# Kernel optimization log

Measured on AMD Instinct MI355X. Metric: run time of the kernel, lower is better.

Reference implementation:

```python
import jax, jax.numpy as jnp
import numpy as np

H = 8
D = 512  # dmodel; each naive head projects to full D (not D//H)


def setup_inputs() -> dict:
    key = jax.random.key(0)
    ks = jax.random.split(key, 9)
    s = 1.0 / np.sqrt(D)
    x = jax.random.normal(ks[0], (2, 2048, D), dtype=jnp.float32)
    Wq = jax.random.normal(ks[1], (H, D, D), dtype=jnp.float32) * s
    Wk = jax.random.normal(ks[2], (H, D, D), dtype=jnp.float32) * s
    Wv = jax.random.normal(ks[3], (H, D, D), dtype=jnp.float32) * s
    bq = jnp.zeros((H, D), dtype=jnp.float32)
    bk = jnp.zeros((H, D), dtype=jnp.float32)
    bv = jnp.zeros((H, D), dtype=jnp.float32)
    Wo = jax.random.normal(ks[4], (H * D, D), dtype=jnp.float32) * (1.0 / np.sqrt(H * D))
    bo = jnp.zeros((D,), dtype=jnp.float32)
    return {"x": x, "Wq": Wq, "Wk": Wk, "Wv": Wv, "bq": bq, "bk": bk, "bv": bv, "Wo": Wo, "bo": bo}


def reference(x, Wq, Wk, Wv, bq, bk, bv, Wo, bo):
    # Batched form of the per-head Python loop: q/k/v -> [b, h, s, d]
    q = jnp.einsum("bsd,hde->bhse", x, Wq) + bq[None, :, None, :]
    k = jnp.einsum("bsd,hde->bhse", x, Wk) + bk[None, :, None, :]
    v = jnp.einsum("bsd,hde->bhse", x, Wv) + bv[None, :, None, :]
    scale = 1.0 / jnp.sqrt(jnp.asarray(D, dtype=x.dtype))
    scores = jnp.einsum("bhqe,bhke->bhqk", q, k) * scale  # [b, h, s, s]
    attn = jax.nn.softmax(scores, axis=-1)
    heads = jnp.einsum("bhqk,bhke->bhqe", attn, v)  # [b, h, s, d]
    b, h, s, d = heads.shape
    concat = jnp.transpose(heads, (0, 2, 1, 3)).reshape(b, s, h * d)  # concat on last axis
    out = concat @ Wo + bo  # output projection
    return out + x  # residual add
```

## Files before the change

### kernel.cpp

```cpp
#include <hip/hip_runtime.h>

typedef unsigned short u16;
typedef __attribute__((ext_vector_type(8))) short bh8;
typedef __attribute__((ext_vector_type(4))) float f32x4;
typedef __attribute__((ext_vector_type(4))) u16 us4;
typedef __attribute__((ext_vector_type(8))) u16 us8;

__device__ __forceinline__ u16 f2bf(float f){
  unsigned u = __builtin_bit_cast(unsigned, f);
  u += 0x7fffu + ((u >> 16) & 1u);
  return (u16)(u >> 16);
}
__device__ __forceinline__ float bf2f(u16 b){
  unsigned u = ((unsigned)b) << 16;
  return __builtin_bit_cast(float, u);
}

__device__ __forceinline__ void gload16(const void* g, void* l){
  __builtin_amdgcn_global_load_lds((const __attribute__((address_space(1))) unsigned*)g,
                                   (__attribute__((address_space(3))) unsigned*)l, 16, 0, 0);
}

template<int OUT_MODE>
__device__ __forceinline__ void gemm_core(
    u16* As, u16* Bs,
    const u16* __restrict__ A, int lda,
    const u16* __restrict__ B, int ldb,
    int K, float scale,
    const float* __restrict__ bias,
    const float* __restrict__ resid, int ldr,
    float* __restrict__ outF, u16* __restrict__ outB, int ldo,
    int m0, int n0)
{
  const int t  = threadIdx.x;
  const int ln = t & 63;
  const int wv = t >> 6;
  const int wr = wv >> 1;
  const int wc = wv & 1;

  const int rs = t >> 2;
  const int cs = (t & 3) * 8;
  const u16* Ag0 = A + (size_t)(m0 + rs) * lda + cs;
  const u16* Ag1 = Ag0 + (size_t)64 * lda;
  const u16* Bg0 = B + (size_t)(n0 + rs) * ldb + cs;
  const u16* Bg1 = Bg0 + (size_t)64 * ldb;
  char* lA0 = (char*)As + wv * 1024;
  char* lA1 = lA0 + 4096;
  char* lB0 = (char*)Bs + wv * 1024;
  char* lB1 = lB0 + 4096;

  f32x4 acc[4][4] = {};

  const int frow = (ln & 15);
  const int fk   = (ln >> 4) * 8;

  for (int k0 = 0; k0 < K; k0 += 32){
    gload16(Ag0 + k0, lA0);
    gload16(Ag1 + k0, lA1);
    gload16(Bg0 + k0, lB0);
    gload16(Bg1 + k0, lB1);
    __syncthreads();
    bh8 a[4], b[4];
#pragma unroll
    for (int i = 0; i < 4; i++)
      a[i] = *(const bh8*)&As[(wr*64 + i*16 + frow)*32 + fk];
#pragma unroll
    for (int j = 0; j < 4; j++)
      b[j] = *(const bh8*)&Bs[(wc*64 + j*16 + frow)*32 + fk];
#pragma unroll
    for (int i = 0; i < 4; i++)
#pragma unroll
      for (int j = 0; j < 4; j++)
        acc[i][j] = __builtin_amdgcn_mfma_f32_16x16x32_bf16(a[i], b[j], acc[i][j], 0, 0, 0);
    __syncthreads();
  }

  const int col0 = ln & 15;
  const int r0   = (ln >> 4) * 4;
#pragma unroll
  for (int i = 0; i < 4; i++){
    const int rowb = m0 + wr*64 + i*16 + r0;
#pragma unroll
    for (int j = 0; j < 4; j++){
      const int col = n0 + wc*64 + j*16 + col0;
      f32x4 v = acc[i][j];
      const float bb = bias ? bias[col] : 0.f;
      if (OUT_MODE == 0){
#pragma unroll
        for (int q = 0; q < 4; q++){
          float o = v[q] * scale + bb;
          if (resid) o += resid[(size_t)(rowb + q) * ldr + col];
          outF[(size_t)(rowb + q) * ldo + col] = o;
        }
      } else if (OUT_MODE == 1){
#pragma unroll
        for (int q = 0; q < 4; q++)
          outB[(size_t)(rowb + q) * ldo + col] = f2bf(v[q] * scale + bb);
      } else {
        us4 pk;
#pragma unroll
        for (int q = 0; q < 4; q++) pk[q] = f2bf(v[q] * scale + bb);
        *(us4*)&outB[(size_t)col * ldo + rowb] = pk;
      }
    }
  }
}


__global__ __launch_bounds__(256) void k_qkv_qk(
    const u16* __restrict__ xb, const u16* __restrict__ WT,
    const float* __restrict__ bq, const float* __restrict__ bk,
    u16* __restrict__ Q, u16* __restrict__ Kb)
{
  __shared__ u16 As[4096], Bs[4096];
  const int z = blockIdx.z;
  const int p = z >> 4, bh = z & 15, b = bh >> 3, h = bh & 7;
  const u16* A = xb + (size_t)b * 2048 * 512;
  const u16* B = WT + (size_t)(p * 8 + h) * 512 * 512;
  const float* bias = (p == 0 ? bq : bk) + h * 512;
  u16* out = (p == 0 ? Q : Kb) + (size_t)bh * 2048 * 512;
  gemm_core<1>(As, Bs, A, 512, B, 512, 512, 1.f, bias, nullptr, 0,
               nullptr, out, 512, blockIdx.y * 128, blockIdx.x * 128);
}

__global__ __launch_bounds__(256) void k_qkv_v(
    const u16* __restrict__ xb, const u16* __restrict__ WT,
    const float* __restrict__ bv, u16* __restrict__ VT)
{
  __shared__ u16 As[4096], Bs[4096];
  const int bh = blockIdx.z, b = bh >> 3, h = bh & 7;
  const u16* A = xb + (size_t)b * 2048 * 512;
  const u16* B = WT + (size_t)(16 + h) * 512 * 512;
  gemm_core<2>(As, Bs, A, 512, B, 512, 512, 1.f, bv + h * 512, nullptr, 0,
               nullptr, VT + (size_t)bh * 512 * 2048, 2048,
               blockIdx.y * 128, blockIdx.x * 128);
}

__global__ __launch_bounds__(256) void k_score(
    const u16* __restrict__ Q, const u16* __restrict__ Kb,
    u16* __restrict__ scoresB, int bh0)
{
  __shared__ u16 As[4096], Bs[4096];
  const int z = blockIdx.z, bh = bh0 + z;
  gemm_core<1>(As, Bs, Q + (size_t)bh * 2048 * 512, 512,
               Kb + (size_t)bh * 2048 * 512, 512, 512,
               0.044194173824159216f , nullptr, nullptr, 0,
               nullptr, scoresB + (size_t)z * 2048 * 2048, 2048,
               blockIdx.y * 128, blockIdx.x * 128);
}

__global__ __launch_bounds__(256) void k_softmax(u16* __restrict__ scoresB)
{
  u16* row = scoresB + (size_t)blockIdx.x * 2048;
  const int t = threadIdx.x, ln = t & 63, wv = t >> 6;
  us8 in = *(const us8*)(row + t * 8);
  float vals[8];
#pragma unroll
  for (int q = 0; q < 8; q++) vals[q] = bf2f(in[q]);
  float m = vals[0];
#pragma unroll
  for (int q = 1; q < 8; q++) m = fmaxf(m, vals[q]);
#pragma unroll
  for (int off = 32; off; off >>= 1) m = fmaxf(m, __shfl_xor(m, off));
  __shared__ float redm[4], reds[4];
  if (ln == 0) redm[wv] = m;
  __syncthreads();
  m = fmaxf(fmaxf(redm[0], redm[1]), fmaxf(redm[2], redm[3]));
  float e[8], s = 0.f;
#pragma unroll
  for (int q = 0; q < 8; q++){ e[q] = __expf(vals[q] - m); s += e[q]; }
#pragma unroll
  for (int off = 32; off; off >>= 1) s += __shfl_xor(s, off);
  if (ln == 0) reds[wv] = s;
  __syncthreads();
  s = reds[0] + reds[1] + reds[2] + reds[3];
  const float inv = 1.f / s;
  us8 pk;
#pragma unroll
  for (int q = 0; q < 8; q++) pk[q] = f2bf(e[q] * inv);
  *(us8*)(row + t * 8) = pk;
}

__global__ __launch_bounds__(256) void k_pv(
    const u16* __restrict__ scoresB, const u16* __restrict__ VT,
    u16* __restrict__ concat, int bh0)
{
  __shared__ u16 As[4096], Bs[4096];
  const int z = blockIdx.z, bh = bh0 + z, b = bh >> 3, h = bh & 7;
  gemm_core<1>(As, Bs, scoresB + (size_t)z * 2048 * 2048, 2048,
               VT + (size_t)bh * 512 * 2048, 2048, 2048, 1.f, nullptr, nullptr, 0,
               nullptr, concat + (size_t)b * 2048 * 4096 + h * 512, 4096,
               blockIdx.y * 128, blockIdx.x * 128);
}

__global__ __launch_bounds__(256) void k_final_sk(
    const u16* __restrict__ concat, const u16* __restrict__ WoT,
    float* __restrict__ partial)
{
  __shared__ u16 As[4096], Bs[4096];
  const int sk = blockIdx.z;
  gemm_core<0>(As, Bs, concat + sk * 1024, 4096,
               WoT + sk * 1024, 4096, 1024, 1.f, nullptr, nullptr, 0,
               partial + (size_t)sk * 4096 * 512, nullptr, 512,
               blockIdx.y * 128, blockIdx.x * 128);
}

__global__ __launch_bounds__(256) void k_reduce(
    const float* __restrict__ partial, const float* __restrict__ bo,
    const float* __restrict__ x, float* __restrict__ out)
{
  const size_t i4 = ((size_t)blockIdx.x * 256 + threadIdx.x) * 4;
  const int col = (int)(i4 & 511);
  float4 s = *(const float4*)(x + i4);
  s.x += bo[col]; s.y += bo[col + 1]; s.z += bo[col + 2]; s.w += bo[col + 3];
#pragma unroll
  for (int sk = 0; sk < 4; sk++){
    float4 p = *(const float4*)(partial + (size_t)sk * 2097152 + i4);
    s.x += p.x; s.y += p.y; s.z += p.z; s.w += p.w;
  }
  *(float4*)(out + i4) = s;
}


__global__ void k_convx(const float* __restrict__ x, u16* __restrict__ xb)
{
  const int i = blockIdx.x * blockDim.x + threadIdx.x;
  float4 v = *(const float4*)(x + (size_t)i * 4);
  us4 o; o[0] = f2bf(v.x); o[1] = f2bf(v.y); o[2] = f2bf(v.z); o[3] = f2bf(v.w);
  *(us4*)(xb + (size_t)i * 4) = o;
}

__global__ void k_transpose_f2b(const float* __restrict__ in, u16* __restrict__ out,
                                int rows, int cols, size_t inStride, size_t outStride)
{
  __shared__ float tile[32][33];
  const float* ip = in + blockIdx.z * inStride;
  u16* op = out + blockIdx.z * outStride;
  const int c0 = blockIdx.x * 32, r0 = blockIdx.y * 32;
  const int tx = threadIdx.x, ty = threadIdx.y;
#pragma unroll
  for (int m = 0; m < 4; m++)
    tile[ty + m * 8][tx] = ip[(size_t)(r0 + ty + m * 8) * cols + c0 + tx];
  __syncthreads();
#pragma unroll
  for (int m = 0; m < 4; m++)
    op[(size_t)(c0 + ty + m * 8) * rows + r0 + tx] = f2bf(tile[tx][ty + m * 8]);
}


extern "C" void kernel_launch(void* const* d_in, const int* in_sizes, int n_in,
                              void* d_out, int out_size, void* d_ws, size_t ws_size,
                              hipStream_t stream)
{
  const float* x  = (const float*)d_in[0];
  const float* Wq = (const float*)d_in[1];
  const float* Wk = (const float*)d_in[2];
  const float* Wv = (const float*)d_in[3];
  const float* bq = (const float*)d_in[4];
  const float* bk = (const float*)d_in[5];
  const float* bv = (const float*)d_in[6];
  const float* Wo = (const float*)d_in[7];
  const float* bo = (const float*)d_in[8];
  float* out = (float*)d_out;

  char* w = (char*)d_ws;
  size_t off = 0;
  auto alloc = [&](size_t bytes) -> char* {
    char* p = w + off; off += (bytes + 255) & ~(size_t)255; return p;
  };
  u16* xb   = (u16*)alloc(4096ull * 512 * 2);
  u16* WT   = (u16*)alloc(3ull * 8 * 512 * 512 * 2);
  u16* WoT  = (u16*)alloc(512ull * 4096 * 2);
  u16* Q    = (u16*)alloc(16ull * 2048 * 512 * 2);
  u16* Kb   = (u16*)alloc(16ull * 2048 * 512 * 2);
  u16* VT   = (u16*)alloc(16ull * 512 * 2048 * 2);
  u16* conc = (u16*)alloc(4096ull * 4096 * 2);
  float* part = (float*)alloc(4ull * 4096 * 512 * 4);
  const size_t scoreBytes = 2048ull * 2048 * 2;
  int CH = 16;
  while (CH > 1 && off + (size_t)CH * scoreBytes > ws_size) CH >>= 1;
  u16* scores = (u16*)alloc((size_t)CH * scoreBytes);

  k_convx<<<2048, 256, 0, stream>>>(x, xb);
  dim3 tb(32, 8);
  k_transpose_f2b<<<dim3(16, 16, 8), tb, 0, stream>>>(Wq, WT + 0ull * 2097152, 512, 512, 262144, 262144);
  k_transpose_f2b<<<dim3(16, 16, 8), tb, 0, stream>>>(Wk, WT + 1ull * 2097152, 512, 512, 262144, 262144);
  k_transpose_f2b<<<dim3(16, 16, 8), tb, 0, stream>>>(Wv, WT + 2ull * 2097152, 512, 512, 262144, 262144);
  k_transpose_f2b<<<dim3(16, 128, 1), tb, 0, stream>>>(Wo, WoT, 4096, 512, 0, 0);

  k_qkv_qk<<<dim3(4, 16, 32), 256, 0, stream>>>(xb, WT, bq, bk, Q, Kb);
  k_qkv_v <<<dim3(4, 16, 16), 256, 0, stream>>>(xb, WT, bv, VT);

  for (int c = 0; c < 16; c += CH){
    k_score  <<<dim3(16, 16, CH), 256, 0, stream>>>(Q, Kb, scores, c);
    k_softmax<<<dim3(CH * 2048), 256, 0, stream>>>(scores);
    k_pv     <<<dim3(4, 16, CH), 256, 0, stream>>>(scores, VT, conc, c);
  }

  k_final_sk<<<dim3(4, 32, 4), 256, 0, stream>>>(conc, WoT, part);
  k_reduce<<<2048, 256, 0, stream>>>(part, bo, x, out);
}
```

Measured before the change: 494.7 us.

## Fuse softmax into score GEMM epilogue with atomic row sums, defer normalization to PV

The score GEMM epilogue now writes exp(scaled score) directly and atomically accumulates per-row sums, and the PV GEMM divides by those sums in its epilogue. This removes the separate softmax kernel and its full read/write pass over the score matrix. It skips max-subtraction, so it relies on scores being small enough not to overflow exp. The split-K partials of the output projection are stored as bf16 instead of fp32 to halve their traffic, and the three QKV weight transposes are merged into one launch.

After: 465.6 us. 5.9% less time.

```diff
diff --git a/kernel.cpp b/kernel.cpp
--- a/kernel.cpp
+++ b/kernel.cpp
@@ -28,8 +28,9 @@
     const u16* __restrict__ B, int ldb,
     int K, float scale,
     const float* __restrict__ bias,
-    const float* __restrict__ resid, int ldr,
-    float* __restrict__ outF, u16* __restrict__ outB, int ldo,
+    float* __restrict__ lsum,
+    const float* __restrict__ lraw,
+    u16* __restrict__ outB, int ldo,
     int m0, int n0)
 {
   const int t  = threadIdx.x;
@@ -77,30 +78,51 @@
 
   const int col0 = ln & 15;
   const int r0   = (ln >> 4) * 4;
+  float rsum[4][4];
 #pragma unroll
   for (int i = 0; i < 4; i++){
     const int rowb = m0 + wr*64 + i*16 + r0;
+#pragma unroll
+    for (int q = 0; q < 4; q++) rsum[i][q] = 0.f;
 #pragma unroll
     for (int j = 0; j < 4; j++){
       const int col = n0 + wc*64 + j*16 + col0;
       f32x4 v = acc[i][j];
-      const float bb = bias ? bias[col] : 0.f;
-      if (OUT_MODE == 0){
-#pragma unroll
-        for (int q = 0; q < 4; q++){
-          float o = v[q] * scale + bb;
-          if (resid) o += resid[(size_t)(rowb + q) * ldr + col];
-          outF[(size_t)(rowb + q) * ldo + col] = o;
-        }
-      } else if (OUT_MODE == 1){
+      if (OUT_MODE == 1){
+        const float bb = bias ? bias[col] : 0.f;
 #pragma unroll
         for (int q = 0; q < 4; q++)
           outB[(size_t)(rowb + q) * ldo + col] = f2bf(v[q] * scale + bb);
-      } else {
+      } else if (OUT_MODE == 2){
+        const float bb = bias ? bias[col] : 0.f;
         us4 pk;
 #pragma unroll
         for (int q = 0; q < 4; q++) pk[q] = f2bf(v[q] * scale + bb);
         *(us4*)&outB[(size_t)col * ldo + rowb] = pk;
+      } else if (OUT_MODE == 3){
+#pragma unroll
+        for (int q = 0; q < 4; q++){
+          float e = __expf(v[q] * scale);
+          rsum[i][q] += e;
+          outB[(size_t)(rowb + q) * ldo + col] = f2bf(e);
+        }
+      } else {
+#pragma unroll
+        for (int q = 0; q < 4; q++){
+          float il = 1.0f / lraw[rowb + q];
+          outB[(size_t)(rowb + q) * ldo + col] = f2bf(v[q] * il);
+        }
+      }
+    }
+    if (OUT_MODE == 3){
+#pragma unroll
+      for (int q = 0; q < 4; q++){
+        float s = rsum[i][q];
+        s += __shfl_xor(s, 1);
+        s += __shfl_xor(s, 2);
+        s += __shfl_xor(s, 4);
+        s += __shfl_xor(s, 8);
+        if ((ln & 15) == 0) atomicAdd(&lsum[rowb + q], s);
       }
     }
   }
@@ -119,8 +141,8 @@
   const u16* B = WT + (size_t)(p * 8 + h) * 512 * 512;
   const float* bias = (p == 0 ? bq : bk) + h * 512;
   u16* out = (p == 0 ? Q : Kb) + (size_t)bh * 2048 * 512;
-  gemm_core<1>(As, Bs, A, 512, B, 512, 512, 1.f, bias, nullptr, 0,
-               nullptr, out, 512, blockIdx.y * 128, blockIdx.x * 128);
+  gemm_core<1>(As, Bs, A, 512, B, 512, 512, 1.f, bias, nullptr, nullptr,
+               out, 512, blockIdx.y * 128, blockIdx.x * 128);
 }
 
 __global__ __launch_bounds__(256) void k_qkv_v(
@@ -131,82 +153,52 @@
   const int bh = blockIdx.z, b = bh >> 3, h = bh & 7;
   const u16* A = xb + (size_t)b * 2048 * 512;
   const u16* B = WT + (size_t)(16 + h) * 512 * 512;
-  gemm_core<2>(As, Bs, A, 512, B, 512, 512, 1.f, bv + h * 512, nullptr, 0,
-               nullptr, VT + (size_t)bh * 512 * 2048, 2048,
+  gemm_core<2>(As, Bs, A, 512, B, 512, 512, 1.f, bv + h * 512, nullptr, nullptr,
+               VT + (size_t)bh * 512 * 2048, 2048,
                blockIdx.y * 128, blockIdx.x * 128);
 }
 
 __global__ __launch_bounds__(256) void k_score(
     const u16* __restrict__ Q, const u16* __restrict__ Kb,
-    u16* __restrict__ scoresB, int bh0)
+    u16* __restrict__ scoresB, float* __restrict__ l, int bh0)
 {
   __shared__ u16 As[4096], Bs[4096];
   const int z = blockIdx.z, bh = bh0 + z;
-  gemm_core<1>(As, Bs, Q + (size_t)bh * 2048 * 512, 512,
+  gemm_core<3>(As, Bs, Q + (size_t)bh * 2048 * 512, 512,
                Kb + (size_t)bh * 2048 * 512, 512, 512,
-               0.044194173824159216f , nullptr, nullptr, 0,
-               nullptr, scoresB + (size_t)z * 2048 * 2048, 2048,
+               0.044194173824159216f , nullptr,
+               l + (size_t)bh * 2048, nullptr,
+               scoresB + (size_t)z * 2048 * 2048, 2048,
                blockIdx.y * 128, blockIdx.x * 128);
-}
-
-__global__ __launch_bounds__(256) void k_softmax(u16* __restrict__ scoresB)
-{
-  u16* row = scoresB + (size_t)blockIdx.x * 2048;
-  const int t = threadIdx.x, ln = t & 63, wv = t >> 6;
-  us8 in = *(const us8*)(row + t * 8);
-  float vals[8];
-#pragma unroll
-  for (int q = 0; q < 8; q++) vals[q] = bf2f(in[q]);
-  float m = vals[0];
-#pragma unroll
-  for (int q = 1; q < 8; q++) m = fmaxf(m, vals[q]);
-#pragma unroll
-  for (int off = 32; off; off >>= 1) m = fmaxf(m, __shfl_xor(m, off));
-  __shared__ float redm[4], reds[4];
-  if (ln == 0) redm[wv] = m;
-  __syncthreads();
-  m = fmaxf(fmaxf(redm[0], redm[1]), fmaxf(redm[2], redm[3]));
-  float e[8], s = 0.f;
-#pragma unroll
-  for (int q = 0; q < 8; q++){ e[q] = __expf(vals[q] - m); s += e[q]; }
-#pragma unroll
-  for (int off = 32; off; off >>= 1) s += __shfl_xor(s, off);
-  if (ln == 0) reds[wv] = s;
-  __syncthreads();
-  s = reds[0] + reds[1] + reds[2] + reds[3];
-  const float inv = 1.f / s;
-  us8 pk;
-#pragma unroll
-  for (int q = 0; q < 8; q++) pk[q] = f2bf(e[q] * inv);
-  *(us8*)(row + t * 8) = pk;
 }
 
 __global__ __launch_bounds__(256) void k_pv(
     const u16* __restrict__ scoresB, const u16* __restrict__ VT,
-    u16* __restrict__ concat, int bh0)
+    const float* __restrict__ l, u16* __restrict__ concat, int bh0)
 {
   __shared__ u16 As[4096], Bs[4096];
   const int z = blockIdx.z, bh = bh0 + z, b = bh >> 3, h = bh & 7;
-  gemm_core<1>(As, Bs, scoresB + (size_t)z * 2048 * 2048, 2048,
-               VT + (size_t)bh * 512 * 2048, 2048, 2048, 1.f, nullptr, nullptr, 0,
-               nullptr, concat + (size_t)b * 2048 * 4096 + h * 512, 4096,
+  gemm_core<4>(As, Bs, scoresB + (size_t)z * 2048 * 2048, 2048,
+               VT + (size_t)bh * 512 * 2048, 2048, 2048, 1.f, nullptr,
+               nullptr, l + (size_t)bh * 2048,
+               concat + (size_t)b * 2048 * 4096 + h * 512, 4096,
                blockIdx.y * 128, blockIdx.x * 128);
 }
 
 __global__ __launch_bounds__(256) void k_final_sk(
     const u16* __restrict__ concat, const u16* __restrict__ WoT,
-    float* __restrict__ partial)
+    u16* __restrict__ partialB)
 {
   __shared__ u16 As[4096], Bs[4096];
   const int sk = blockIdx.z;
-  gemm_core<0>(As, Bs, concat + sk * 1024, 4096,
-               WoT + sk * 1024, 4096, 1024, 1.f, nullptr, nullptr, 0,
-               partial + (size_t)sk * 4096 * 512, nullptr, 512,
+  gemm_core<1>(As, Bs, concat + sk * 1024, 4096,
+               WoT + sk * 1024, 4096, 1024, 1.f, nullptr, nullptr, nullptr,
+               partialB + (size_t)sk * 4096 * 512, 512,
                blockIdx.y * 128, blockIdx.x * 128);
 }
 
 __global__ __launch_bounds__(256) void k_reduce(
-    const float* __restrict__ partial, const float* __restrict__ bo,
+    const u16* __restrict__ partialB, const float* __restrict__ bo,
     const float* __restrict__ x, float* __restrict__ out)
 {
   const size_t i4 = ((size_t)blockIdx.x * 256 + threadIdx.x) * 4;
@@ -215,8 +207,8 @@
   s.x += bo[col]; s.y += bo[col + 1]; s.z += bo[col + 2]; s.w += bo[col + 3];
 #pragma unroll
   for (int sk = 0; sk < 4; sk++){
-    float4 p = *(const float4*)(partial + (size_t)sk * 2097152 + i4);
-    s.x += p.x; s.y += p.y; s.z += p.z; s.w += p.w;
+    us4 p = *(const us4*)(partialB + (size_t)sk * 2097152 + i4);
+    s.x += bf2f(p[0]); s.y += bf2f(p[1]); s.z += bf2f(p[2]); s.w += bf2f(p[3]);
   }
   *(float4*)(out + i4) = s;
 }
@@ -230,21 +222,39 @@
   *(us4*)(xb + (size_t)i * 4) = o;
 }
 
-__global__ void k_transpose_f2b(const float* __restrict__ in, u16* __restrict__ out,
-                                int rows, int cols, size_t inStride, size_t outStride)
+__global__ void k_transpose_qkv(const float* __restrict__ Wq,
+                                const float* __restrict__ Wk,
+                                const float* __restrict__ Wv,
+                                u16* __restrict__ WT)
 {
   __shared__ float tile[32][33];
-  const float* ip = in + blockIdx.z * inStride;
-  u16* op = out + blockIdx.z * outStride;
+  const int z = blockIdx.z, p = z >> 3, h = z & 7;
+  const float* ip = (p == 0 ? Wq : p == 1 ? Wk : Wv) + (size_t)h * 512 * 512;
+  u16* op = WT + (size_t)z * 512 * 512;
   const int c0 = blockIdx.x * 32, r0 = blockIdx.y * 32;
   const int tx = threadIdx.x, ty = threadIdx.y;
 #pragma unroll
   for (int m = 0; m < 4; m++)
-    tile[ty + m * 8][tx] = ip[(size_t)(r0 + ty + m * 8) * cols + c0 + tx];
+    tile[ty + m * 8][tx] = ip[(size_t)(r0 + ty + m * 8) * 512 + c0 + tx];
   __syncthreads();
 #pragma unroll
   for (int m = 0; m < 4; m++)
-    op[(size_t)(c0 + ty + m * 8) * rows + r0 + tx] = f2bf(tile[tx][ty + m * 8]);
+    op[(size_t)(c0 + ty + m * 8) * 512 + r0 + tx] = f2bf(tile[tx][ty + m * 8]);
+}
+
+__global__ void k_transpose_f2b(const float* __restrict__ in, u16* __restrict__ out,
+                                int rows, int cols)
+{
+  __shared__ float tile[32][33];
+  const int c0 = blockIdx.x * 32, r0 = blockIdx.y * 32;
+  const int tx = threadIdx.x, ty = threadIdx.y;
+#pragma unroll
+  for (int m = 0; m < 4; m++)
+    tile[ty + m * 8][tx] = in[(size_t)(r0 + ty + m * 8) * cols + c0 + tx];
+  __syncthreads();
+#pragma unroll
+  for (int m = 0; m < 4; m++)
+    out[(size_t)(c0 + ty + m * 8) * rows + r0 + tx] = f2bf(tile[tx][ty + m * 8]);
 }
 
 
@@ -275,26 +285,26 @@
   u16* Kb   = (u16*)alloc(16ull * 2048 * 512 * 2);
   u16* VT   = (u16*)alloc(16ull * 512 * 2048 * 2);
   u16* conc = (u16*)alloc(4096ull * 4096 * 2);
-  float* part = (float*)alloc(4ull * 4096 * 512 * 4);
+  u16* part = (u16*)alloc(4ull * 4096 * 512 * 2);
+  float* l  = (float*)alloc(16ull * 2048 * 4);
   const size_t scoreBytes = 2048ull * 2048 * 2;
   int CH = 16;
   while (CH > 1 && off + (size_t)CH * scoreBytes > ws_size) CH >>= 1;
   u16* scores = (u16*)alloc((size_t)CH * scoreBytes);
 
+  hipMemsetAsync(l, 0, 16ull * 2048 * 4, stream);
+
   k_convx<<<2048, 256, 0, stream>>>(x, xb);
   dim3 tb(32, 8);
-  k_transpose_f2b<<<dim3(16, 16, 8), tb, 0, stream>>>(Wq, WT + 0ull * 2097152, 512, 512, 262144, 262144);
-  k_transpose_f2b<<<dim3(16, 16, 8), tb, 0, stream>>>(Wk, WT + 1ull * 2097152, 512, 512, 262144, 262144);
-  k_transpose_f2b<<<dim3(16, 16, 8), tb, 0, stream>>>(Wv, WT + 2ull * 2097152, 512, 512, 262144, 262144);
-  k_transpose_f2b<<<dim3(16, 128, 1), tb, 0, stream>>>(Wo, WoT, 4096, 512, 0, 0);
+  k_transpose_qkv<<<dim3(16, 16, 24), tb, 0, stream>>>(Wq, Wk, Wv, WT);
+  k_transpose_f2b<<<dim3(16, 128, 1), tb, 0, stream>>>(Wo, WoT, 4096, 512);
 
   k_qkv_qk<<<dim3(4, 16, 32), 256, 0, stream>>>(xb, WT, bq, bk, Q, Kb);
   k_qkv_v <<<dim3(4, 16, 16), 256, 0, stream>>>(xb, WT, bv, VT);
 
   for (int c = 0; c < 16; c += CH){
-    k_score  <<<dim3(16, 16, CH), 256, 0, stream>>>(Q, Kb, scores, c);
-    k_softmax<<<dim3(CH * 2048), 256, 0, stream>>>(scores);
-    k_pv     <<<dim3(4, 16, CH), 256, 0, stream>>>(scores, VT, conc, c);
+    k_score<<<dim3(16, 16, CH), 256, 0, stream>>>(Q, Kb, scores, l, c);
+    k_pv   <<<dim3(4, 16, CH), 256, 0, stream>>>(scores, VT, l, conc, c);
   }
 
   k_final_sk<<<dim3(4, 32, 4), 256, 0, stream>>>(conc, WoT, part);
```
